# Kernel tuning notes

Hardware: AMD Instinct MI355X
Metric: run time of the kernel (lower is better)

The kernel has to match this reference:

```python
import jax, jax.numpy as jnp
import numpy as np
from jax import lax

D_MODEL = 1024
D_STATE = 1024  # must equal D_MODEL due to u*B elementwise multiply in selective_scan
D_CONV = 4
BATCH = 4
SEQ = 4096


def setup_inputs() -> dict:
    key = jax.random.key(0)
    ks = jax.random.split(key, 12)
    s = 0.02
    return {
        "x": jax.random.normal(ks[0], (BATCH, SEQ, D_MODEL), jnp.float32),
        "ln_g": jnp.ones((D_MODEL,), jnp.float32),
        "ln_b": jnp.zeros((D_MODEL,), jnp.float32),
        "w_in": jax.random.normal(ks[1], (2 * D_MODEL, D_MODEL), jnp.float32) * s,
        "b_in": jnp.zeros((2 * D_MODEL,), jnp.float32),
        "w_conv": jax.random.normal(ks[2], (D_MODEL, 1, D_CONV), jnp.float32) * 0.2,
        "b_conv": jnp.zeros((D_MODEL,), jnp.float32),
        "w_delta": jax.random.normal(ks[3], (D_STATE, D_MODEL), jnp.float32) * s,
        "b_delta": jnp.zeros((D_STATE,), jnp.float32),
        "w_B": jax.random.normal(ks[4], (D_STATE, D_MODEL), jnp.float32) * s,
        "b_B": jnp.zeros((D_STATE,), jnp.float32),
        "w_C": jax.random.normal(ks[5], (D_STATE, D_MODEL), jnp.float32) * s,
        "b_C": jnp.zeros((D_STATE,), jnp.float32),
        "w_out": jax.random.normal(ks[6], (D_MODEL, D_MODEL), jnp.float32) * s,
        "b_out": jnp.zeros((D_MODEL,), jnp.float32),
    }


def reference(x, ln_g, ln_b, w_in, b_in, w_conv, b_conv,
              w_delta, b_delta, w_B, b_B, w_C, b_C, w_out, b_out):
    eps = 1e-5
    # LayerNorm
    mu = jnp.mean(x, axis=-1, keepdims=True)
    var = jnp.mean(jnp.square(x - mu), axis=-1, keepdims=True)
    h = (x - mu) * lax.rsqrt(var + eps) * ln_g + ln_b
    # in_proj and chunk
    uv = h @ w_in.T + b_in  # [B, L, 2D]
    u, v = jnp.split(uv, 2, axis=-1)
    # depthwise causal conv1d: torch pads both sides by K-1 then slices [:L] -> left pad only
    K = w_conv.shape[-1]
    u_c = lax.conv_general_dilated(
        u.transpose(0, 2, 1), w_conv, window_strides=(1,),
        padding=[(K - 1, 0)], feature_group_count=u.shape[-1],
        dimension_numbers=("NCH", "OIH", "NCH"))
    u_c = u_c.transpose(0, 2, 1) + b_conv  # [B, L, D]
    # projections
    delta = jax.nn.softplus(u_c @ w_delta.T + b_delta)  # [B, L, N]
    Bm = u_c @ w_B.T + b_B                              # [B, L, N]
    Cm = u_c @ w_C.T + b_C                              # [B, L, N]
    # selective scan: A = -1 broadcast over d_state
    decay = jnp.exp(-delta)        # exp(delta * A)
    inp = u_c * Bm                 # requires d_model == d_state

    def step(hst, t):
        d_t, i_t, c_t = t
        hst = hst * d_t + i_t
        return hst, jnp.sum(hst * c_t, axis=-1)  # [B]

    h0 = jnp.zeros((x.shape[0], Bm.shape[-1]), x.dtype)
    _, ys = lax.scan(step, h0,
                     (decay.transpose(1, 0, 2), inp.transpose(1, 0, 2), Cm.transpose(1, 0, 2)))
    y = ys.T[..., None]            # [B, L, 1]
    y = y * jax.nn.sigmoid(v)      # broadcast to [B, L, D]
    out = y @ w_out.T + b_out
    return x + out
```

## Files before the change

kernel.cpp:

```cpp
#include <hip/hip_runtime.h>
#include <stdint.h>

#define D_MODEL 1024
#define KDIM 1024
#define BATCH 4
#define SEQ 4096
#define MROWS (BATCH*SEQ)
#define CHUNK 64
#define NCHUNK (SEQ/CHUNK)

typedef unsigned short u16;
typedef __attribute__((ext_vector_type(8))) short short8;
typedef __attribute__((ext_vector_type(4))) float f32x4;
typedef __attribute__((ext_vector_type(4))) unsigned short u16x4;

__device__ __forceinline__ u16 f2bf(float f){
  uint32_t b = __builtin_bit_cast(uint32_t, f);
  b += 0x7FFFu + ((b >> 16) & 1u);
  return (u16)(b >> 16);
}
__device__ __forceinline__ float bf2f(u16 u){
  uint32_t b = ((uint32_t)u) << 16;
  return __builtin_bit_cast(float, b);
}

__global__ __launch_bounds__(256) void prep_kernel(
    const float* __restrict__ w_in, const float* __restrict__ w_delta,
    const float* __restrict__ w_B, const float* __restrict__ w_C,
    const float* __restrict__ w_out,
    const float* __restrict__ b_delta, const float* __restrict__ b_B,
    const float* __restrict__ b_C,
    u16* __restrict__ w_in_bf, u16* __restrict__ wcat_bf,
    u16* __restrict__ w_out_bf, float* __restrict__ bcat){
  int i4 = blockIdx.x * 256 + threadIdx.x;
  const float* src; u16* dst; int off;
  if      (i4 <  524288){ src = w_in;    dst = w_in_bf;           off = i4; }
  else if (i4 <  786432){ src = w_delta; dst = wcat_bf;           off = i4 -  524288; }
  else if (i4 < 1048576){ src = w_B;     dst = wcat_bf + 1048576; off = i4 -  786432; }
  else if (i4 < 1310720){ src = w_C;     dst = wcat_bf + 2097152; off = i4 - 1048576; }
  else if (i4 < 1572864){ src = w_out;   dst = w_out_bf;          off = i4 - 1310720; }
  else {
    int t = i4 - 1572864;
    if      (t < 256){ *(float4*)(bcat +        t*4)        = *(const float4*)(b_delta + t*4); }
    else if (t < 512){ *(float4*)(bcat + 1024 + (t-256)*4)  = *(const float4*)(b_B + (t-256)*4); }
    else if (t < 768){ *(float4*)(bcat + 2048 + (t-512)*4)  = *(const float4*)(b_C + (t-512)*4); }
    return;
  }
  float4 v = *(const float4*)(src + (size_t)off * 4);
  u16x4 o; o.x = f2bf(v.x); o.y = f2bf(v.y); o.z = f2bf(v.z); o.w = f2bf(v.w);
  *(u16x4*)(dst + (size_t)off * 4) = o;
}

__global__ __launch_bounds__(256) void ln_kernel(const float* __restrict__ x,
    const float* __restrict__ g, const float* __restrict__ b, u16* __restrict__ h){
  int row = blockIdx.x;
  int tid = threadIdx.x, lane = tid & 63, wid = tid >> 6;
  const float* xr = x + (size_t)row * D_MODEL;
  float4 v = *(const float4*)(xr + tid * 4);
  float s  = v.x + v.y + v.z + v.w;
  float s2 = v.x*v.x + v.y*v.y + v.z*v.z + v.w*v.w;
#pragma unroll
  for (int off = 32; off > 0; off >>= 1){ s += __shfl_down(s, off); s2 += __shfl_down(s2, off); }
  __shared__ float red[8];
  if (lane == 0){ red[wid] = s; red[4 + wid] = s2; }
  __syncthreads();
  s  = red[0] + red[1] + red[2] + red[3];
  s2 = red[4] + red[5] + red[6] + red[7];
  float mu  = s * (1.f / D_MODEL);
  float var = s2 * (1.f / D_MODEL) - mu * mu;
  float rs  = rsqrtf(var + 1e-5f);
  int c = tid * 4;
  u16x4 o;
  o.x = f2bf((v.x - mu) * rs * g[c+0] + b[c+0]);
  o.y = f2bf((v.y - mu) * rs * g[c+1] + b[c+1]);
  o.z = f2bf((v.z - mu) * rs * g[c+2] + b[c+2]);
  o.w = f2bf((v.w - mu) * rs * g[c+3] + b[c+3]);
  *(u16x4*)(h + (size_t)row * D_MODEL + c) = o;
}

#define VMCNT_(N) asm volatile("s_waitcnt vmcnt(" #N ")" ::: "memory")
#define VMCNT(N) VMCNT_(N)

template<int EPI>
__global__ __launch_bounds__(512, 2) void gemm256(
    const u16* __restrict__ A, const u16* __restrict__ W,
    const float* __restrict__ bias,
    u16* __restrict__ outb, float* __restrict__ outf,
    const float* __restrict__ resid, int N){
  __shared__ char lds[131072];
  const int tid = threadIdx.x, wid = tid >> 6, lane = tid & 63;
  const int wm = wid >> 2, wn = wid & 3;
  const int lrow = lane & 15, khi = lane >> 4;

  int nwg = gridDim.x;
  int cpx = nwg >> 3;
  int bid = blockIdx.x;
  int wg = (bid & 7) * cpx + (bid >> 3);
  int ntile = N >> 8;
  int by = wg / ntile, bx = wg % ntile;
  int m0 = by << 8, n0 = bx << 8;

  f32x4 acc[8][4];
  f32x4 zero = {0.f, 0.f, 0.f, 0.f};
#pragma unroll
  for (int i = 0; i < 8; i++)
#pragma unroll
    for (int j = 0; j < 4; j++) acc[i][j] = zero;

  const int xr = ((lrow >> 1) & 3) << 4;
  const int aOff = (wm * 128 + lrow) * 64 + ((khi * 16) ^ xr);
  const int bOff = (wn * 64  + lrow) * 64 + ((khi * 16) ^ xr);

  const int rS = tid >> 2;
  const int cbS = ((tid & 3) * 16) ^ (((rS >> 1) & 3) << 4);
  const u16* gA = A + (size_t)(m0 + rS) * KDIM + (cbS >> 1);
  const u16* gB = W + (size_t)(n0 + rS) * KDIM + (cbS >> 1);

  auto stA = [&](int kt, int bi){
    const u16* g0 = gA + kt;
    unsigned l0 = (unsigned)(bi * 16384 + wid * 1024);
    __builtin_amdgcn_global_load_lds((const __attribute__((address_space(1))) void*)g0,
                                     (__attribute__((address_space(3))) void*)(lds + l0), 16, 0, 0);
    __builtin_amdgcn_global_load_lds((const __attribute__((address_space(1))) void*)(g0 + 128 * KDIM),
                                     (__attribute__((address_space(3))) void*)(lds + l0 + 8192), 16, 0, 0);
  };
  auto stB = [&](int kt, int bi){
    const u16* g0 = gB + kt;
    unsigned l0 = (unsigned)(65536 + bi * 16384 + wid * 1024);
    __builtin_amdgcn_global_load_lds((const __attribute__((address_space(1))) void*)g0,
                                     (__attribute__((address_space(3))) void*)(lds + l0), 16, 0, 0);
    __builtin_amdgcn_global_load_lds((const __attribute__((address_space(1))) void*)(g0 + 128 * KDIM),
                                     (__attribute__((address_space(3))) void*)(lds + l0 + 8192), 16, 0, 0);
  };

#define TILE(BI, STKT, DOSTAGE, WAITC) { \
  const char* pa = lds + (BI) * 16384; \
  const char* pb = lds + 65536 + (BI) * 16384; \
  short8 bfr[4], afr[8]; \
  _Pragma("unroll") \
  for (int nf = 0; nf < 4; nf++) bfr[nf] = *(const short8*)(pb + bOff + nf * 1024); \
  _Pragma("unroll") \
  for (int mi = 0; mi < 8; mi++) afr[mi] = *(const short8*)(pa + aOff + mi * 1024); \
  if (DOSTAGE){ stA((STKT), ((BI) + 3) & 3); stB((STKT), ((BI) + 3) & 3); } \
  __builtin_amdgcn_sched_barrier(0); \
  __builtin_amdgcn_s_setprio(1); \
  _Pragma("unroll") \
  for (int mi = 0; mi < 8; mi++) \
    _Pragma("unroll") \
    for (int nf = 0; nf < 4; nf++) \
      acc[mi][nf] = __builtin_amdgcn_mfma_f32_16x16x32_bf16(afr[mi], bfr[nf], acc[mi][nf], 0, 0, 0); \
  __builtin_amdgcn_s_setprio(0); \
  WAITC; \
  __builtin_amdgcn_s_barrier(); \
}

  stA(0, 0);  stB(0, 0);
  stA(32, 1); stB(32, 1);
  stA(64, 2); stB(64, 2);
  VMCNT(8);
  __builtin_amdgcn_s_barrier();

  for (int kk = 0; kk < 28; kk += 4){
    TILE(0, (kk + 3) << 5, 1, VMCNT(8));
    TILE(1, (kk + 4) << 5, 1, VMCNT(8));
    TILE(2, (kk + 5) << 5, 1, VMCNT(8));
    TILE(3, (kk + 6) << 5, 1, VMCNT(8));
  }
  TILE(0, 992, 1, VMCNT(8));
  TILE(1, 0, 0, VMCNT(4));
  TILE(2, 0, 0, VMCNT(0));
  TILE(3, 0, 0, (void)0);
#undef TILE

  float bv[4];
#pragma unroll
  for (int nf = 0; nf < 4; nf++) bv[nf] = bias[n0 + wn * 64 + nf * 16 + lrow];
#pragma unroll
  for (int mf = 0; mf < 8; mf++){
    int r0 = m0 + wm * 128 + mf * 16 + khi * 4;
#pragma unroll
    for (int nf = 0; nf < 4; nf++){
      int c = n0 + wn * 64 + nf * 16 + lrow;
#pragma unroll
      for (int i2 = 0; i2 < 4; i2++){
        float val = acc[mf][nf][i2] + bv[nf];
        size_t o = (size_t)(r0 + i2) * N + c;
        if (EPI == 0) outb[o] = f2bf(val);
        else          outf[o] = val + resid[o];
      }
    }
  }
}

__global__ __launch_bounds__(256) void conv_kernel(const u16* __restrict__ uv,
    const float* __restrict__ wc, const float* __restrict__ bc, u16* __restrict__ uc){
  int idx = blockIdx.x * 256 + threadIdx.x;
  int d0 = (idx & 127) * 8;
  int m0 = (idx >> 7) * 16;
  int l0 = m0 & (SEQ - 1);
  float4 wv[8]; float bias[8];
#pragma unroll
  for (int j = 0; j < 8; j++){ wv[j] = *(const float4*)(wc + (d0 + j) * 4); bias[j] = bc[d0 + j]; }
  short8 zero8 = {0,0,0,0,0,0,0,0};
  short8 w0 = zero8, w1 = zero8, w2 = zero8;
  if (l0 > 0){
    w0 = *(const short8*)(uv + (size_t)(m0 - 3) * 2048 + d0);
    w1 = *(const short8*)(uv + (size_t)(m0 - 2) * 2048 + d0);
    w2 = *(const short8*)(uv + (size_t)(m0 - 1) * 2048 + d0);
  }
  const u16* pi = uv + (size_t)m0 * 2048 + d0;
  u16* po = uc + (size_t)m0 * 1024 + d0;
#pragma unroll 4
  for (int t = 0; t < 16; t++){
    short8 cur = *(const short8*)pi;  pi += 2048;
    short8 o;
#pragma unroll
    for (int j = 0; j < 8; j++){
      float a = bias[j] + bf2f((u16)w0[j]) * wv[j].x + bf2f((u16)w1[j]) * wv[j].y
                        + bf2f((u16)w2[j]) * wv[j].z + bf2f((u16)cur[j]) * wv[j].w;
      o[j] = (short)f2bf(a);
    }
    *(short8*)po = o;  po += 1024;
    w0 = w1; w1 = w2; w2 = cur;
  }
}

__global__ __launch_bounds__(256) void scanA(const u16* __restrict__ dbc, const u16* __restrict__ uc,
                                             float* __restrict__ P, float* __restrict__ S){
  int idx = blockIdx.x * 256 + threadIdx.x;
  int n0 = (idx & 255) * 4;
  int c = (idx >> 8) & (NCHUNK - 1);
  int b = idx >> 14;
  size_t mbase = (size_t)b * SEQ + c * CHUNK;
  float Pv[4] = {1.f,1.f,1.f,1.f}, Sv[4] = {0.f,0.f,0.f,0.f};
  const u16* pd = dbc + mbase * 3072 + n0;
  const u16* pu = uc + mbase * 1024 + n0;
#pragma unroll 4
  for (int t = 0; t < CHUNK; t++){
    u16x4 dr = *(const u16x4*)pd;
    u16x4 bm = *(const u16x4*)(pd + 1024);
    u16x4 uu = *(const u16x4*)pu;
    pd += 3072; pu += 1024;
#pragma unroll
    for (int j = 0; j < 4; j++){
      float dec = 1.f / (1.f + __expf(bf2f(dr[j])));
      Pv[j] *= dec;
      Sv[j] = Sv[j] * dec + bf2f(uu[j]) * bf2f(bm[j]);
    }
  }
  int o = (b * NCHUNK + c) * 1024 + n0;
  float4 p4 = {Pv[0], Pv[1], Pv[2], Pv[3]};
  float4 s4 = {Sv[0], Sv[1], Sv[2], Sv[3]};
  *(float4*)(P + o) = p4;
  *(float4*)(S + o) = s4;
}

__global__ void scanB(const float* __restrict__ P, const float* __restrict__ S,
                      float* __restrict__ Hin){
  int idx = blockIdx.x * 256 + threadIdx.x;
  int n0 = (idx & 255) * 4, b = idx >> 8;
  float4 H = {0.f,0.f,0.f,0.f};
  for (int c = 0; c < NCHUNK; c++){
    int o = (b * NCHUNK + c) * 1024 + n0;
    *(float4*)(Hin + o) = H;
    float4 p = *(const float4*)(P + o);
    float4 s = *(const float4*)(S + o);
    H.x = H.x * p.x + s.x;  H.y = H.y * p.y + s.y;
    H.z = H.z * p.z + s.z;  H.w = H.w * p.w + s.w;
  }
}

__global__ __launch_bounds__(256) void scanC(const u16* __restrict__ dbc, const u16* __restrict__ uc,
                                             const float* __restrict__ Hin,
                                             const u16* __restrict__ uv, u16* __restrict__ gg){
  int b = blockIdx.x >> 6, c = blockIdx.x & (NCHUNK - 1);
  int tid = threadIdx.x;
  int n0 = tid * 4;
  __shared__ float part[CHUNK][257];
  __shared__ float red2[CHUNK][5];
  __shared__ float ys[CHUNK];
  size_t mbase = (size_t)b * SEQ + c * CHUNK;
  float4 h4 = *(const float4*)(Hin + (b * NCHUNK + c) * 1024 + n0);
  float h[4] = {h4.x, h4.y, h4.z, h4.w};
  const u16* pd = dbc + mbase * 3072 + n0;
  const u16* pu = uc + mbase * 1024 + n0;
#pragma unroll 2
  for (int t = 0; t < CHUNK; t++){
    u16x4 dr = *(const u16x4*)pd;
    u16x4 bm = *(const u16x4*)(pd + 1024);
    u16x4 cm = *(const u16x4*)(pd + 2048);
    u16x4 uu = *(const u16x4*)pu;
    pd += 3072; pu += 1024;
    float contrib = 0.f;
#pragma unroll
    for (int j = 0; j < 4; j++){
      float dec = 1.f / (1.f + __expf(bf2f(dr[j])));
      h[j] = h[j] * dec + bf2f(uu[j]) * bf2f(bm[j]);
      contrib += h[j] * bf2f(cm[j]);
    }
    part[t][tid] = contrib;
  }
  __syncthreads();
  {
    int t = tid & 63, q = tid >> 6;
    float s = 0.f;
#pragma unroll
    for (int j = 0; j < 64; j++) s += part[t][q * 64 + j];
    red2[t][q] = s;
  }
  __syncthreads();
  if (tid < CHUNK) ys[tid] = red2[tid][0] + red2[tid][1] + red2[tid][2] + red2[tid][3];
  __syncthreads();
  const u16* pv = uv + mbase * 2048 + 1024;
  u16* pg = gg + mbase * 1024;
#pragma unroll 4
  for (int i2 = 0; i2 < 32; i2++){
    int e = i2 * 256 + tid;
    int t = e >> 7, ch = e & 127;
    short8 v = *(const short8*)(pv + (size_t)t * 2048 + ch * 8);
    float yv = ys[t];
    short8 o;
#pragma unroll
    for (int j = 0; j < 8; j++){
      float vf = bf2f((u16)v[j]);
      float sg = 1.f / (1.f + __expf(-vf));
      o[j] = (short)f2bf(yv * sg);
    }
    *(short8*)(pg + (size_t)t * 1024 + ch * 8) = o;
  }
}

extern "C" void kernel_launch(void* const* d_in, const int* in_sizes, int n_in,
                              void* d_out, int out_size, void* d_ws, size_t ws_size,
                              hipStream_t stream) {
  const float* x      = (const float*)d_in[0];
  const float* ln_g   = (const float*)d_in[1];
  const float* ln_b   = (const float*)d_in[2];
  const float* w_in   = (const float*)d_in[3];
  const float* b_in   = (const float*)d_in[4];
  const float* w_conv = (const float*)d_in[5];
  const float* b_conv = (const float*)d_in[6];
  const float* w_delta= (const float*)d_in[7];
  const float* b_delta= (const float*)d_in[8];
  const float* w_B    = (const float*)d_in[9];
  const float* b_B    = (const float*)d_in[10];
  const float* w_C    = (const float*)d_in[11];
  const float* b_C    = (const float*)d_in[12];
  const float* w_out  = (const float*)d_in[13];
  const float* b_out  = (const float*)d_in[14];

  char* w = (char*)d_ws;
  u16* w_in_bf  = (u16*)w; w += (size_t)2 * 1024 * 1024 * 2;
  u16* wcat_bf  = (u16*)w; w += (size_t)3 * 1024 * 1024 * 2;
  u16* w_out_bf = (u16*)w; w += (size_t)1024 * 1024 * 2;
  float* bcat   = (float*)w; w += 16384;
  u16* h_bf     = (u16*)w; w += (size_t)MROWS * 1024 * 2;
  u16* uv_bf    = (u16*)w; w += (size_t)MROWS * 2048 * 2;
  u16* uc_bf    = (u16*)w; w += (size_t)MROWS * 1024 * 2;
  u16* dbc_bf   = (u16*)w; w += (size_t)MROWS * 3072 * 2;
  float* P      = (float*)w; w += (size_t)BATCH * NCHUNK * 1024 * 4;
  float* S      = (float*)w; w += (size_t)BATCH * NCHUNK * 1024 * 4;
  float* Hin    = (float*)w; w += (size_t)BATCH * NCHUNK * 1024 * 4;
  u16* gg       = h_bf;

  prep_kernel<<<6147, 256, 0, stream>>>(w_in, w_delta, w_B, w_C, w_out,
                                        b_delta, b_B, b_C,
                                        w_in_bf, wcat_bf, w_out_bf, bcat);

  ln_kernel<<<MROWS, 256, 0, stream>>>(x, ln_g, ln_b, h_bf);

  gemm256<0><<<dim3((2048/256) * (MROWS/256)), 512, 0, stream>>>(
      h_bf, w_in_bf, b_in, uv_bf, nullptr, nullptr, 2048);

  conv_kernel<<<(MROWS / 16) * 128 / 256, 256, 0, stream>>>(uv_bf, w_conv, b_conv, uc_bf);

  gemm256<0><<<dim3((3072/256) * (MROWS/256)), 512, 0, stream>>>(
      uc_bf, wcat_bf, bcat, dbc_bf, nullptr, nullptr, 3072);

  scanA<<<(BATCH * NCHUNK * 1024 / 4) / 256, 256, 0, stream>>>(dbc_bf, uc_bf, P, S);
  scanB<<<(BATCH * 1024 / 4) / 256, 256, 0, stream>>>(P, S, Hin);
  scanC<<<BATCH * NCHUNK, 256, 0, stream>>>(dbc_bf, uc_bf, Hin, uv_bf, gg);

  gemm256<1><<<dim3((1024/256) * (MROWS/256)), 512, 0, stream>>>(
      gg, w_out_bf, b_out, nullptr, (float*)d_out, x, 1024);
}
```

Measured before the change: 347.1 us.

## Double-buffer MFMA register fragments to prefetch next LDS tile during compute

The GEMM main loop now keeps two sets of A/B register fragments and loads the next K-tile's fragments from LDS before issuing the current tile's MFMAs, rather than reading and then immediately consuming them. The aim is to hide LDS read latency behind matrix instructions. The vmcnt waits are tightened so the next buffer is resident one stage earlier, which shortens the global-load prefetch slack. Doubling the fragment registers raises VGPR pressure and may lower occupancy.

```diff
diff --git a/kernel.cpp b/kernel.cpp
--- a/kernel.cpp
+++ b/kernel.cpp
@@ -133,14 +133,17 @@
                                      (__attribute__((address_space(3))) void*)(lds + l0 + 8192), 16, 0, 0);
   };
 
-#define TILE(BI, STKT, DOSTAGE, WAITC) { \
-  const char* pa = lds + (BI) * 16384; \
-  const char* pb = lds + 65536 + (BI) * 16384; \
-  short8 bfr[4], afr[8]; \
-  _Pragma("unroll") \
-  for (int nf = 0; nf < 4; nf++) bfr[nf] = *(const short8*)(pb + bOff + nf * 1024); \
-  _Pragma("unroll") \
-  for (int mi = 0; mi < 8; mi++) afr[mi] = *(const short8*)(pa + aOff + mi * 1024); \
+  short8 afrA[8], bfrA[4], afrB[8], bfrB[4];
+
+#define TILE(BI, CA, CB, NA, NB, RDNEXT, STKT, DOSTAGE, WAITC) { \
+  if (RDNEXT){ \
+    const char* pa = lds + ((((BI) + 1) & 3) * 16384); \
+    const char* pb = lds + 65536 + ((((BI) + 1) & 3) * 16384); \
+    _Pragma("unroll") \
+    for (int nf = 0; nf < 4; nf++) NB[nf] = *(const short8*)(pb + bOff + nf * 1024); \
+    _Pragma("unroll") \
+    for (int mi = 0; mi < 8; mi++) NA[mi] = *(const short8*)(pa + aOff + mi * 1024); \
+  } \
   if (DOSTAGE){ stA((STKT), ((BI) + 3) & 3); stB((STKT), ((BI) + 3) & 3); } \
   __builtin_amdgcn_sched_barrier(0); \
   __builtin_amdgcn_s_setprio(1); \
@@ -148,7 +151,7 @@
   for (int mi = 0; mi < 8; mi++) \
     _Pragma("unroll") \
     for (int nf = 0; nf < 4; nf++) \
-      acc[mi][nf] = __builtin_amdgcn_mfma_f32_16x16x32_bf16(afr[mi], bfr[nf], acc[mi][nf], 0, 0, 0); \
+      acc[mi][nf] = __builtin_amdgcn_mfma_f32_16x16x32_bf16(CA[mi], CB[nf], acc[mi][nf], 0, 0, 0); \
   __builtin_amdgcn_s_setprio(0); \
   WAITC; \
   __builtin_amdgcn_s_barrier(); \
@@ -157,19 +160,27 @@
   stA(0, 0);  stB(0, 0);
   stA(32, 1); stB(32, 1);
   stA(64, 2); stB(64, 2);
-  VMCNT(8);
+  VMCNT(4);
   __builtin_amdgcn_s_barrier();
+  {
+    const char* pa = lds;
+    const char* pb = lds + 65536;
+#pragma unroll
+    for (int nf = 0; nf < 4; nf++) bfrA[nf] = *(const short8*)(pb + bOff + nf * 1024);
+#pragma unroll
+    for (int mi = 0; mi < 8; mi++) afrA[mi] = *(const short8*)(pa + aOff + mi * 1024);
+  }
 
   for (int kk = 0; kk < 28; kk += 4){
-    TILE(0, (kk + 3) << 5, 1, VMCNT(8));
-    TILE(1, (kk + 4) << 5, 1, VMCNT(8));
-    TILE(2, (kk + 5) << 5, 1, VMCNT(8));
-    TILE(3, (kk + 6) << 5, 1, VMCNT(8));
-  }
-  TILE(0, 992, 1, VMCNT(8));
-  TILE(1, 0, 0, VMCNT(4));
-  TILE(2, 0, 0, VMCNT(0));
-  TILE(3, 0, 0, (void)0);
+    TILE(0, afrA, bfrA, afrB, bfrB, 1, (kk + 3) << 5, 1, VMCNT(4));
+    TILE(1, afrB, bfrB, afrA, bfrA, 1, (kk + 4) << 5, 1, VMCNT(4));
+    TILE(2, afrA, bfrA, afrB, bfrB, 1, (kk + 5) << 5, 1, VMCNT(4));
+    TILE(3, afrB, bfrB, afrA, bfrA, 1, (kk + 6) << 5, 1, VMCNT(4));
+  }
+  TILE(0, afrA, bfrA, afrB, bfrB, 1, 992, 1, VMCNT(4));
+  TILE(1, afrB, bfrB, afrA, bfrA, 1, 0, 0, VMCNT(0));
+  TILE(2, afrA, bfrA, afrB, bfrB, 1, 0, 0, (void)0);
+  TILE(3, afrB, bfrB, afrA, bfrA, 0, 0, 0, (void)0);
 #undef TILE
 
   float bv[4];
```

Result: slower. 365.2 us (+5.2%).

## Load GEMM B operand directly from global into registers, halving LDS use

Applied to the files above, without the earlier changes.

The B (weight) tile is no longer staged through LDS. Each wave loads its B fragments straight from global memory into double-buffered registers one k-step ahead, and A keeps the 4-stage LDS pipeline. This halves shared memory per block, which could allow more occupancy, and removes the LDS traffic for B. In exchange, each wave issues uncoalesced 16-byte global loads that other waves duplicate, and global latency is exposed with only one tile of lookahead. The vmcnt bookkeeping becomes more fragile.

```diff
diff --git a/kernel.cpp b/kernel.cpp
--- a/kernel.cpp
+++ b/kernel.cpp
@@ -87,7 +87,7 @@
     const float* __restrict__ bias,
     u16* __restrict__ outb, float* __restrict__ outf,
     const float* __restrict__ resid, int N){
-  __shared__ char lds[131072];
+  __shared__ char lds[65536];
   const int tid = threadIdx.x, wid = tid >> 6, lane = tid & 63;
   const int wm = wid >> 2, wn = wid & 3;
   const int lrow = lane & 15, khi = lane >> 4;
@@ -109,12 +109,12 @@
 
   const int xr = ((lrow >> 1) & 3) << 4;
   const int aOff = (wm * 128 + lrow) * 64 + ((khi * 16) ^ xr);
-  const int bOff = (wn * 64  + lrow) * 64 + ((khi * 16) ^ xr);
 
   const int rS = tid >> 2;
   const int cbS = ((tid & 3) * 16) ^ (((rS >> 1) & 3) << 4);
   const u16* gA = A + (size_t)(m0 + rS) * KDIM + (cbS >> 1);
-  const u16* gB = W + (size_t)(n0 + rS) * KDIM + (cbS >> 1);
+
+  const u16* gBd = W + (size_t)(n0 + wn * 64 + lrow) * KDIM + khi * 8;
 
   auto stA = [&](int kt, int bi){
     const u16* g0 = gA + kt;
@@ -124,52 +124,49 @@
     __builtin_amdgcn_global_load_lds((const __attribute__((address_space(1))) void*)(g0 + 128 * KDIM),
                                      (__attribute__((address_space(3))) void*)(lds + l0 + 8192), 16, 0, 0);
   };
-  auto stB = [&](int kt, int bi){
-    const u16* g0 = gB + kt;
-    unsigned l0 = (unsigned)(65536 + bi * 16384 + wid * 1024);
-    __builtin_amdgcn_global_load_lds((const __attribute__((address_space(1))) void*)g0,
-                                     (__attribute__((address_space(3))) void*)(lds + l0), 16, 0, 0);
-    __builtin_amdgcn_global_load_lds((const __attribute__((address_space(1))) void*)(g0 + 128 * KDIM),
-                                     (__attribute__((address_space(3))) void*)(lds + l0 + 8192), 16, 0, 0);
-  };
-
-#define TILE(BI, STKT, DOSTAGE, WAITC) { \
+
+  short8 Bs0[4], Bs1[4];
+
+#define TILE(BI, CURB, STKT, DOSTAGE, BKT, DOLDB, WAITC) { \
   const char* pa = lds + (BI) * 16384; \
-  const char* pb = lds + 65536 + (BI) * 16384; \
-  short8 bfr[4], afr[8]; \
-  _Pragma("unroll") \
-  for (int nf = 0; nf < 4; nf++) bfr[nf] = *(const short8*)(pb + bOff + nf * 1024); \
+  short8 afr[8]; \
   _Pragma("unroll") \
   for (int mi = 0; mi < 8; mi++) afr[mi] = *(const short8*)(pa + aOff + mi * 1024); \
-  if (DOSTAGE){ stA((STKT), ((BI) + 3) & 3); stB((STKT), ((BI) + 3) & 3); } \
+  if (DOSTAGE){ stA((STKT), ((BI) + 3) & 3); } \
   __builtin_amdgcn_sched_barrier(0); \
   __builtin_amdgcn_s_setprio(1); \
   _Pragma("unroll") \
   for (int mi = 0; mi < 8; mi++) \
     _Pragma("unroll") \
     for (int nf = 0; nf < 4; nf++) \
-      acc[mi][nf] = __builtin_amdgcn_mfma_f32_16x16x32_bf16(afr[mi], bfr[nf], acc[mi][nf], 0, 0, 0); \
+      acc[mi][nf] = __builtin_amdgcn_mfma_f32_16x16x32_bf16(afr[mi], CURB[nf], acc[mi][nf], 0, 0, 0); \
   __builtin_amdgcn_s_setprio(0); \
+  if (DOLDB){ \
+    _Pragma("unroll") \
+    for (int nf = 0; nf < 4; nf++) CURB[nf] = *(const short8*)(gBd + (BKT) + nf * 16384); \
+  } \
   WAITC; \
   __builtin_amdgcn_s_barrier(); \
 }
 
-  stA(0, 0);  stB(0, 0);
-  stA(32, 1); stB(32, 1);
-  stA(64, 2); stB(64, 2);
-  VMCNT(8);
+  stA(0, 0); stA(32, 1); stA(64, 2);
+#pragma unroll
+  for (int nf = 0; nf < 4; nf++) Bs0[nf] = *(const short8*)(gBd +  0 + nf * 16384);
+#pragma unroll
+  for (int nf = 0; nf < 4; nf++) Bs1[nf] = *(const short8*)(gBd + 32 + nf * 16384);
+  VMCNT(4);
   __builtin_amdgcn_s_barrier();
 
   for (int kk = 0; kk < 28; kk += 4){
-    TILE(0, (kk + 3) << 5, 1, VMCNT(8));
-    TILE(1, (kk + 4) << 5, 1, VMCNT(8));
-    TILE(2, (kk + 5) << 5, 1, VMCNT(8));
-    TILE(3, (kk + 6) << 5, 1, VMCNT(8));
-  }
-  TILE(0, 992, 1, VMCNT(8));
-  TILE(1, 0, 0, VMCNT(4));
-  TILE(2, 0, 0, VMCNT(0));
-  TILE(3, 0, 0, (void)0);
+    TILE(0, Bs0, (kk + 3) << 5, 1, (kk + 2) << 5, 1, VMCNT(6));
+    TILE(1, Bs1, (kk + 4) << 5, 1, (kk + 3) << 5, 1, VMCNT(6));
+    TILE(2, Bs0, (kk + 5) << 5, 1, (kk + 4) << 5, 1, VMCNT(6));
+    TILE(3, Bs1, (kk + 6) << 5, 1, (kk + 5) << 5, 1, VMCNT(6));
+  }
+  TILE(0, Bs0, 31 << 5, 1, 30 << 5, 1, VMCNT(6));
+  TILE(1, Bs1, 0, 0, 31 << 5, 1, VMCNT(4));
+  TILE(2, Bs0, 0, 0, 0, 0, VMCNT(0));
+  TILE(3, Bs1, 0, 0, 0, 0, (void)0);
 #undef TILE
 
   float bv[4];
```

New measurement: 446.5 us. +28.6%, slower.

## Split scan output into local and carry terms; fuse weight prep with LayerNorm

Applied to the files above, without the earlier changes.

The chunked scan is reformulated. scanA now computes, in one pass, the chunk-local output contribution (ylocal) and a per-step cumulative-decay times C vector (G, stored bf16 in the h buffer). scanC then only needs a dot product of the incoming carry state with G plus ylocal, so it no longer re-reads dbc and uc or recomputes exponentials. The weight conversion and LayerNorm kernels are merged into a single launch. The cost is a bf16 G intermediate, which adds rounding error and extra writes.

```diff
diff --git a/kernel.cpp b/kernel.cpp
--- a/kernel.cpp
+++ b/kernel.cpp
@@ -24,14 +24,42 @@
   return __builtin_bit_cast(float, b);
 }
 
-__global__ __launch_bounds__(256) void prep_kernel(
+__global__ __launch_bounds__(256) void prep_ln_kernel(
     const float* __restrict__ w_in, const float* __restrict__ w_delta,
     const float* __restrict__ w_B, const float* __restrict__ w_C,
     const float* __restrict__ w_out,
     const float* __restrict__ b_delta, const float* __restrict__ b_B,
     const float* __restrict__ b_C,
     u16* __restrict__ w_in_bf, u16* __restrict__ wcat_bf,
-    u16* __restrict__ w_out_bf, float* __restrict__ bcat){
+    u16* __restrict__ w_out_bf, float* __restrict__ bcat,
+    const float* __restrict__ x, const float* __restrict__ g,
+    const float* __restrict__ bb, u16* __restrict__ h){
+  if (blockIdx.x >= 6147){
+    int row = blockIdx.x - 6147;
+    int tid = threadIdx.x, lane = tid & 63, wid = tid >> 6;
+    const float* xr = x + (size_t)row * D_MODEL;
+    float4 v = *(const float4*)(xr + tid * 4);
+    float s  = v.x + v.y + v.z + v.w;
+    float s2 = v.x*v.x + v.y*v.y + v.z*v.z + v.w*v.w;
+#pragma unroll
+    for (int off = 32; off > 0; off >>= 1){ s += __shfl_down(s, off); s2 += __shfl_down(s2, off); }
+    __shared__ float red[8];
+    if (lane == 0){ red[wid] = s; red[4 + wid] = s2; }
+    __syncthreads();
+    s  = red[0] + red[1] + red[2] + red[3];
+    s2 = red[4] + red[5] + red[6] + red[7];
+    float mu  = s * (1.f / D_MODEL);
+    float var = s2 * (1.f / D_MODEL) - mu * mu;
+    float rs  = rsqrtf(var + 1e-5f);
+    int c = tid * 4;
+    u16x4 o;
+    o.x = f2bf((v.x - mu) * rs * g[c+0] + bb[c+0]);
+    o.y = f2bf((v.y - mu) * rs * g[c+1] + bb[c+1]);
+    o.z = f2bf((v.z - mu) * rs * g[c+2] + bb[c+2]);
+    o.w = f2bf((v.w - mu) * rs * g[c+3] + bb[c+3]);
+    *(u16x4*)(h + (size_t)row * D_MODEL + c) = o;
+    return;
+  }
   int i4 = blockIdx.x * 256 + threadIdx.x;
   const float* src; u16* dst; int off;
   if      (i4 <  524288){ src = w_in;    dst = w_in_bf;           off = i4; }
@@ -49,33 +77,6 @@
   float4 v = *(const float4*)(src + (size_t)off * 4);
   u16x4 o; o.x = f2bf(v.x); o.y = f2bf(v.y); o.z = f2bf(v.z); o.w = f2bf(v.w);
   *(u16x4*)(dst + (size_t)off * 4) = o;
-}
-
-__global__ __launch_bounds__(256) void ln_kernel(const float* __restrict__ x,
-    const float* __restrict__ g, const float* __restrict__ b, u16* __restrict__ h){
-  int row = blockIdx.x;
-  int tid = threadIdx.x, lane = tid & 63, wid = tid >> 6;
-  const float* xr = x + (size_t)row * D_MODEL;
-  float4 v = *(const float4*)(xr + tid * 4);
-  float s  = v.x + v.y + v.z + v.w;
-  float s2 = v.x*v.x + v.y*v.y + v.z*v.z + v.w*v.w;
-#pragma unroll
-  for (int off = 32; off > 0; off >>= 1){ s += __shfl_down(s, off); s2 += __shfl_down(s2, off); }
-  __shared__ float red[8];
-  if (lane == 0){ red[wid] = s; red[4 + wid] = s2; }
-  __syncthreads();
-  s  = red[0] + red[1] + red[2] + red[3];
-  s2 = red[4] + red[5] + red[6] + red[7];
-  float mu  = s * (1.f / D_MODEL);
-  float var = s2 * (1.f / D_MODEL) - mu * mu;
-  float rs  = rsqrtf(var + 1e-5f);
-  int c = tid * 4;
-  u16x4 o;
-  o.x = f2bf((v.x - mu) * rs * g[c+0] + b[c+0]);
-  o.y = f2bf((v.y - mu) * rs * g[c+1] + b[c+1]);
-  o.z = f2bf((v.z - mu) * rs * g[c+2] + b[c+2]);
-  o.w = f2bf((v.w - mu) * rs * g[c+3] + b[c+3]);
-  *(u16x4*)(h + (size_t)row * D_MODEL + c) = o;
 }
 
 #define VMCNT_(N) asm volatile("s_waitcnt vmcnt(" #N ")" ::: "memory")
@@ -226,28 +227,49 @@
 }
 
 __global__ __launch_bounds__(256) void scanA(const u16* __restrict__ dbc, const u16* __restrict__ uc,
-                                             float* __restrict__ P, float* __restrict__ S){
-  int idx = blockIdx.x * 256 + threadIdx.x;
-  int n0 = (idx & 255) * 4;
-  int c = (idx >> 8) & (NCHUNK - 1);
-  int b = idx >> 14;
+                                             u16* __restrict__ G, float* __restrict__ P,
+                                             float* __restrict__ S, float* __restrict__ ylocal){
+  int b = blockIdx.x >> 6, c = blockIdx.x & (NCHUNK - 1);
+  int tid = threadIdx.x, n0 = tid * 4;
+  __shared__ float part[CHUNK][257];
+  __shared__ float red2[CHUNK][5];
   size_t mbase = (size_t)b * SEQ + c * CHUNK;
   float Pv[4] = {1.f,1.f,1.f,1.f}, Sv[4] = {0.f,0.f,0.f,0.f};
   const u16* pd = dbc + mbase * 3072 + n0;
   const u16* pu = uc + mbase * 1024 + n0;
-#pragma unroll 4
+  u16* pg = G + mbase * 1024 + n0;
+#pragma unroll 2
   for (int t = 0; t < CHUNK; t++){
     u16x4 dr = *(const u16x4*)pd;
     u16x4 bm = *(const u16x4*)(pd + 1024);
+    u16x4 cm = *(const u16x4*)(pd + 2048);
     u16x4 uu = *(const u16x4*)pu;
     pd += 3072; pu += 1024;
+    float contrib = 0.f;
+    u16x4 go;
 #pragma unroll
     for (int j = 0; j < 4; j++){
       float dec = 1.f / (1.f + __expf(bf2f(dr[j])));
+      float cf = bf2f(cm[j]);
       Pv[j] *= dec;
       Sv[j] = Sv[j] * dec + bf2f(uu[j]) * bf2f(bm[j]);
+      go[j] = f2bf(Pv[j] * cf);
+      contrib += Sv[j] * cf;
     }
-  }
+    *(u16x4*)pg = go;  pg += 1024;
+    part[t][tid] = contrib;
+  }
+  __syncthreads();
+  {
+    int t = tid & 63, q = tid >> 6;
+    float s = 0.f;
+#pragma unroll
+    for (int j = 0; j < 64; j++) s += part[t][q * 64 + j];
+    red2[t][q] = s;
+  }
+  __syncthreads();
+  if (tid < CHUNK)
+    ylocal[mbase + tid] = red2[tid][0] + red2[tid][1] + red2[tid][2] + red2[tid][3];
   int o = (b * NCHUNK + c) * 1024 + n0;
   float4 p4 = {Pv[0], Pv[1], Pv[2], Pv[3]};
   float4 s4 = {Sv[0], Sv[1], Sv[2], Sv[3]};
@@ -270,35 +292,22 @@
   }
 }
 
-__global__ __launch_bounds__(256) void scanC(const u16* __restrict__ dbc, const u16* __restrict__ uc,
-                                             const float* __restrict__ Hin,
-                                             const u16* __restrict__ uv, u16* __restrict__ gg){
+__global__ __launch_bounds__(256) void scanC(u16* gbuf, const float* __restrict__ Hin,
+                                             const float* __restrict__ ylocal,
+                                             const u16* __restrict__ uv){
   int b = blockIdx.x >> 6, c = blockIdx.x & (NCHUNK - 1);
-  int tid = threadIdx.x;
-  int n0 = tid * 4;
+  int tid = threadIdx.x, n0 = tid * 4;
   __shared__ float part[CHUNK][257];
   __shared__ float red2[CHUNK][5];
   __shared__ float ys[CHUNK];
   size_t mbase = (size_t)b * SEQ + c * CHUNK;
   float4 h4 = *(const float4*)(Hin + (b * NCHUNK + c) * 1024 + n0);
-  float h[4] = {h4.x, h4.y, h4.z, h4.w};
-  const u16* pd = dbc + mbase * 3072 + n0;
-  const u16* pu = uc + mbase * 1024 + n0;
-#pragma unroll 2
+  const u16* pG = gbuf + mbase * 1024 + n0;
+#pragma unroll 4
   for (int t = 0; t < CHUNK; t++){
-    u16x4 dr = *(const u16x4*)pd;
-    u16x4 bm = *(const u16x4*)(pd + 1024);
-    u16x4 cm = *(const u16x4*)(pd + 2048);
-    u16x4 uu = *(const u16x4*)pu;
-    pd += 3072; pu += 1024;
-    float contrib = 0.f;
-#pragma unroll
-    for (int j = 0; j < 4; j++){
-      float dec = 1.f / (1.f + __expf(bf2f(dr[j])));
-      h[j] = h[j] * dec + bf2f(uu[j]) * bf2f(bm[j]);
-      contrib += h[j] * bf2f(cm[j]);
-    }
-    part[t][tid] = contrib;
+    u16x4 g = *(const u16x4*)pG;  pG += 1024;
+    part[t][tid] = h4.x * bf2f(g.x) + h4.y * bf2f(g.y)
+                 + h4.z * bf2f(g.z) + h4.w * bf2f(g.w);
   }
   __syncthreads();
   {
@@ -309,10 +318,11 @@
     red2[t][q] = s;
   }
   __syncthreads();
-  if (tid < CHUNK) ys[tid] = red2[tid][0] + red2[tid][1] + red2[tid][2] + red2[tid][3];
+  if (tid < CHUNK)
+    ys[tid] = red2[tid][0] + red2[tid][1] + red2[tid][2] + red2[tid][3] + ylocal[mbase + tid];
   __syncthreads();
   const u16* pv = uv + mbase * 2048 + 1024;
-  u16* pg = gg + mbase * 1024;
+  u16* pg = gbuf + mbase * 1024;
 #pragma unroll 4
   for (int i2 = 0; i2 < 32; i2++){
     int e = i2 * 256 + tid;
@@ -361,13 +371,12 @@
   float* P      = (float*)w; w += (size_t)BATCH * NCHUNK * 1024 * 4;
   float* S      = (float*)w; w += (size_t)BATCH * NCHUNK * 1024 * 4;
   float* Hin    = (float*)w; w += (size_t)BATCH * NCHUNK * 1024 * 4;
-  u16* gg       = h_bf;
-
-  prep_kernel<<<6147, 256, 0, stream>>>(w_in, w_delta, w_B, w_C, w_out,
-                                        b_delta, b_B, b_C,
-                                        w_in_bf, wcat_bf, w_out_bf, bcat);
-
-  ln_kernel<<<MROWS, 256, 0, stream>>>(x, ln_g, ln_b, h_bf);
+  float* ylocal = (float*)w; w += (size_t)MROWS * 4;
+  u16* gbuf     = h_bf;
+
+  prep_ln_kernel<<<6147 + MROWS, 256, 0, stream>>>(
+      w_in, w_delta, w_B, w_C, w_out, b_delta, b_B, b_C,
+      w_in_bf, wcat_bf, w_out_bf, bcat, x, ln_g, ln_b, h_bf);
 
   gemm256<0><<<dim3((2048/256) * (MROWS/256)), 512, 0, stream>>>(
       h_bf, w_in_bf, b_in, uv_bf, nullptr, nullptr, 2048);
@@ -377,10 +386,10 @@
   gemm256<0><<<dim3((3072/256) * (MROWS/256)), 512, 0, stream>>>(
       uc_bf, wcat_bf, bcat, dbc_bf, nullptr, nullptr, 3072);
 
-  scanA<<<(BATCH * NCHUNK * 1024 / 4) / 256, 256, 0, stream>>>(dbc_bf, uc_bf, P, S);
+  scanA<<<BATCH * NCHUNK, 256, 0, stream>>>(dbc_bf, uc_bf, gbuf, P, S, ylocal);
   scanB<<<(BATCH * 1024 / 4) / 256, 256, 0, stream>>>(P, S, Hin);
-  scanC<<<BATCH * NCHUNK, 256, 0, stream>>>(dbc_bf, uc_bf, Hin, uv_bf, gg);
+  scanC<<<BATCH * NCHUNK, 256, 0, stream>>>(gbuf, Hin, ylocal, uv_bf);
 
   gemm256<1><<<dim3((1024/256) * (MROWS/256)), 512, 0, stream>>>(
-      gg, w_out_bf, b_out, nullptr, (float*)d_out, x, 1024);
-}
+      gbuf, w_out_bf, b_out, nullptr, (float*)d_out, x, 1024);
+}
```

After: 333.1 us. -4.0%, faster.
